# Kernel optimization log

Measured on AMD Instinct MI355X. Metric: run time of the kernel, lower is better.

Reference implementation:

```python
import jax, jax.numpy as jnp
import numpy as np

B, N, H, D = 1024, 128, 128, 8  # batch, num_nodes (= num variables), hidden, diffusion size


def setup_inputs() -> dict:
    key = jax.random.key(0)
    ks = jax.random.split(key, 7)
    return {
        "x": jax.random.normal(ks[0], (B, N), dtype=jnp.float32),
        "f_weight": jax.random.normal(ks[1], (N, N, H), dtype=jnp.float32) * 0.1,
        "g_weight": jax.random.normal(ks[2], (N, N, H, D), dtype=jnp.float32) * 0.1,
        "Wf": jax.random.normal(ks[3], (N, H), dtype=jnp.float32) * (1.0 / np.sqrt(H)),
        "bf": jax.random.normal(ks[4], (N,), dtype=jnp.float32) * 0.01,
        "Wg": jax.random.normal(ks[5], (N, H), dtype=jnp.float32) * (1.0 / np.sqrt(H)),
        "bg": jax.random.normal(ks[6], (N,), dtype=jnp.float32) * 0.01,
    }


def reference(x, f_weight, g_weight, Wf, bf, Wg, bg):
    # Drift f: per node i, temp_i = x @ f_weight[i]  -> [B,H]; out_i = fc_i(elu(temp_i)) -> [B,1]
    # Batched over nodes as a single einsum instead of the original Python loop.
    temp_f = jnp.einsum('bn,inh->bih', x, f_weight)              # [B,N,H]
    f_out = jnp.einsum('bih,ih->bi', jax.nn.elu(temp_f), Wf) + bf  # [B,N]

    # Diffusion g: per node i, temp_i = x @ g_weight[i] -> [B,H,D]; fc_i applied over H per diffusion channel.
    temp_g = jnp.einsum('bn,inhd->bihd', x, g_weight)            # [B,N,H,D]
    g_out = jnp.einsum('bihd,ih->bid', jax.nn.elu(temp_g), Wg) + bg[None, :, None]  # [B,N,D]
    return f_out, g_out
```

## Files before the change

### kernel.cpp

```cpp
#include <hip/hip_runtime.h>
#include <hip/hip_bf16.h>


typedef unsigned short u16;
typedef __attribute__((ext_vector_type(8))) short bf16x8;
typedef __attribute__((ext_vector_type(8))) short short8;
typedef __attribute__((ext_vector_type(4))) float f32x4;

typedef __attribute__((address_space(1))) const void* gas_ptr;
typedef __attribute__((address_space(3))) void* las_ptr;
#define GLOAD_LDS16(g, l) __builtin_amdgcn_global_load_lds((gas_ptr)(g), (las_ptr)(l), 16, 0, 0)

#define WS_W_ELEMS  ((size_t)128 * 1152 * 128)
#define WS_X_ELEMS  ((size_t)1024 * 128)
#define WS_NEED_BYTES ((WS_W_ELEMS + WS_X_ELEMS) * 2)

__device__ __forceinline__ u16 f2bf(float f) {
    unsigned int u = __float_as_uint(f);
    u += 0x7fffu + ((u >> 16) & 1u);
    return (u16)(u >> 16);
}
__device__ __forceinline__ uint32_t pack2bf(float a, float b) {
    return (uint32_t)f2bf(a) | ((uint32_t)f2bf(b) << 16);
}
__device__ __forceinline__ float elu(float v) {
    return v > 0.f ? v : __expf(v) - 1.f;
}

__global__ void sde_prepass(const float* __restrict__ fw, const float* __restrict__ gw,
                            const float* __restrict__ x, u16* __restrict__ wsW) {
    const int bx = blockIdx.x;
    const int t  = threadIdx.x;
    if (bx < 8192) {
        const int i  = bx >> 6;
        const int c  = (((bx >> 4) & 3) << 8) + t;
        const int n0 = (bx & 15) << 3;
        const float* src = gw + (size_t)i * 131072;
        float v[8];
        #pragma unroll
        for (int j = 0; j < 8; ++j) v[j] = src[(size_t)(n0 + j) * 1024 + c];
        short8 o;
        #pragma unroll
        for (int j = 0; j < 8; ++j) o[j] = (short)f2bf(v[j]);
        *(short8*)&wsW[((size_t)i * 1152 + c) * 128 + n0] = o;
    } else if (bx < 9216) {
        const int b2 = bx - 8192;
        const int i  = b2 >> 3;
        const int c  = t & 127;
        const int n0 = (((b2 & 7) << 1) + (t >> 7)) << 3;
        const float* src = fw + (size_t)i * 16384;
        float v[8];
        #pragma unroll
        for (int j = 0; j < 8; ++j) v[j] = src[(size_t)(n0 + j) * 128 + c];
        short8 o;
        #pragma unroll
        for (int j = 0; j < 8; ++j) o[j] = (short)f2bf(v[j]);
        *(short8*)&wsW[((size_t)i * 1152 + 1024 + c) * 128 + n0] = o;
    } else {
        const int tid = (bx - 9216) * 256 + t;
        float4 v = ((const float4*)x)[tid];
        ((uint2*)(wsW + WS_W_ELEMS))[tid] = make_uint2(pack2bf(v.x, v.y), pack2bf(v.z, v.w));
    }
}

__global__ __launch_bounds__(256, 4) void sde_mfma(
    const u16* __restrict__ wsAll,
    const float* __restrict__ Wf, const float* __restrict__ bfp,
    const float* __restrict__ Wg, const float* __restrict__ bgp,
    float* __restrict__ out)
{
    __shared__ u16 wst[64 * 128];
    __shared__ float wgs[128];
    __shared__ float wfs[128];

    const int t    = threadIdx.x;
    const int bx   = blockIdx.x;
    const int i    = bx & 127;
    const int b0   = (bx >> 7) << 7;
    const int w    = t >> 6;
    const int lane = t & 63;
    const int l15  = lane & 15;
    const int quad = lane >> 4;
    const int rl   = lane >> 4;
    const int j16  = lane & 15;
    const int sw   = l15 & 7;

    const u16* wsW = wsAll;
    const u16* wsX = wsAll + WS_W_ELEMS;

    if (t < 128) { wgs[t] = Wg[i * 128 + t]; wfs[t] = Wf[i * 128 + t]; }

    bf16x8 afrag[2][4];
    {
        const size_t r0 = (size_t)(b0 + w * 32 + l15) * 128 + quad * 8;
        #pragma unroll
        for (int kk = 0; kk < 4; ++kk) {
            afrag[0][kk] = *(const bf16x8*)&wsX[r0 + kk * 32];
            afrag[1][kk] = *(const bf16x8*)&wsX[r0 + 16 * 128 + kk * 32];
        }
    }

    float racc[8], frac[8];
    #pragma unroll
    for (int q = 0; q < 8; ++q) { racc[q] = 0.f; frac[q] = 0.f; }

    for (int ct = 0; ct < 18; ++ct) {
        {
            const char* srcW = (const char*)(wsW + ((size_t)i * 1152 + ct * 64) * 128);
            #pragma unroll
            for (int r = 0; r < 4; ++r) {
                int row = w * 16 + r * 4 + rl;
                int soff = row * 256 + ((j16 ^ (row & 7)) << 4);
                GLOAD_LDS16(srcW + soff, (char*)wst + w * 4096 + r * 1024);
            }
        }
        __syncthreads();

        f32x4 acc[2][4];
        #pragma unroll
        for (int rs = 0; rs < 2; ++rs)
            #pragma unroll
            for (int cs = 0; cs < 4; ++cs)
                acc[rs][cs] = (f32x4){0.f, 0.f, 0.f, 0.f};

        #pragma unroll
        for (int kk = 0; kk < 4; ++kk) {
            const int co = ((kk * 4 + quad) ^ sw) << 3;
            bf16x8 bv[4];
            #pragma unroll
            for (int cs = 0; cs < 4; ++cs)
                bv[cs] = *(const bf16x8*)&wst[(cs * 16 + l15) * 128 + co];
            #pragma unroll
            for (int cs = 0; cs < 4; ++cs) {
                acc[0][cs] = __builtin_amdgcn_mfma_f32_16x16x32_bf16(afrag[0][kk], bv[cs], acc[0][cs], 0, 0, 0);
                acc[1][cs] = __builtin_amdgcn_mfma_f32_16x16x32_bf16(afrag[1][kk], bv[cs], acc[1][cs], 0, 0, 0);
            }
        }

        if (ct < 16) {
            float wv[4];
            #pragma unroll
            for (int cs = 0; cs < 4; ++cs) wv[cs] = wgs[ct * 8 + cs * 2 + (l15 >> 3)];
            #pragma unroll
            for (int rs = 0; rs < 2; ++rs)
                #pragma unroll
                for (int rg = 0; rg < 4; ++rg) {
                    racc[rs * 4 + rg] += elu(acc[rs][0][rg]) * wv[0] + elu(acc[rs][1][rg]) * wv[1]
                                       + elu(acc[rs][2][rg]) * wv[2] + elu(acc[rs][3][rg]) * wv[3];
                }
        } else {
            float wv[4];
            #pragma unroll
            for (int cs = 0; cs < 4; ++cs) wv[cs] = wfs[(ct - 16) * 64 + cs * 16 + l15];
            #pragma unroll
            for (int rs = 0; rs < 2; ++rs)
                #pragma unroll
                for (int rg = 0; rg < 4; ++rg) {
                    frac[rs * 4 + rg] += elu(acc[rs][0][rg]) * wv[0] + elu(acc[rs][1][rg]) * wv[1]
                                       + elu(acc[rs][2][rg]) * wv[2] + elu(acc[rs][3][rg]) * wv[3];
                }
        }
        __syncthreads();
    }

    const float bfv = bfp[i], bgv = bgp[i];
    #pragma unroll
    for (int rs = 0; rs < 2; ++rs)
        #pragma unroll
        for (int rg = 0; rg < 4; ++rg) {
            int q = rs * 4 + rg;
            racc[q] += __shfl_xor(racc[q], 8);
            float fsum = frac[q];
            fsum += __shfl_xor(fsum, 1);
            fsum += __shfl_xor(fsum, 2);
            fsum += __shfl_xor(fsum, 4);
            fsum += __shfl_xor(fsum, 8);
            int row = w * 32 + rs * 16 + quad * 4 + rg;
            size_t brow = (size_t)(b0 + row);
            if (l15 == 0)
                out[brow * 128 + i] = fsum + bfv;
            if (l15 < 8)
                out[(size_t)131072 + (brow * 128 + i) * 8 + (lane & 7)] = racc[q] + bgv;
        }
}

__global__ void sde_fallback(const float* __restrict__ x, const float* __restrict__ fw,
                             const float* __restrict__ gw,
                             const float* __restrict__ Wf, const float* __restrict__ bfp,
                             const float* __restrict__ Wg, const float* __restrict__ bgp,
                             float* __restrict__ out)
{
    __shared__ float xsh[64 * 128];
    const int t  = threadIdx.x;
    const int i  = blockIdx.x >> 4;
    const int b0 = (blockIdx.x & 15) << 6;
    for (int idx = t; idx < 64 * 128; idx += 64) xsh[idx] = x[(size_t)b0 * 128 + idx];
    __syncthreads();
    const float* xr  = &xsh[t * 128];
    const float* fwi = fw + (size_t)i * 16384;
    const float* gwi = gw + (size_t)i * 131072;
    float fa = 0.f;
    for (int h = 0; h < 128; ++h) {
        float tf = 0.f;
        for (int n = 0; n < 128; ++n) tf += xr[n] * fwi[n * 128 + h];
        fa += elu(tf) * Wf[i * 128 + h];
    }
    float ga[8];
    #pragma unroll
    for (int d = 0; d < 8; ++d) ga[d] = 0.f;
    for (int h = 0; h < 128; ++h) {
        float tg[8] = {0, 0, 0, 0, 0, 0, 0, 0};
        for (int n = 0; n < 128; ++n) {
            float xv = xr[n];
            const float* gp = gwi + ((size_t)n * 128 + h) * 8;
            #pragma unroll
            for (int d = 0; d < 8; ++d) tg[d] += xv * gp[d];
        }
        float wv = Wg[i * 128 + h];
        #pragma unroll
        for (int d = 0; d < 8; ++d) ga[d] += elu(tg[d]) * wv;
    }
    size_t b = (size_t)(b0 + t);
    out[b * 128 + i] = fa + bfp[i];
    #pragma unroll
    for (int d = 0; d < 8; ++d)
        out[(size_t)131072 + (b * 128 + i) * 8 + d] = ga[d] + bgp[i];
}

extern "C" void kernel_launch(void* const* d_in, const int* in_sizes, int n_in,
                              void* d_out, int out_size, void* d_ws, size_t ws_size,
                              hipStream_t stream) {
    const float* x  = (const float*)d_in[0];
    const float* fw = (const float*)d_in[1];
    const float* gw = (const float*)d_in[2];
    const float* Wf = (const float*)d_in[3];
    const float* bf = (const float*)d_in[4];
    const float* Wg = (const float*)d_in[5];
    const float* bg = (const float*)d_in[6];
    float* out = (float*)d_out;

    if (ws_size >= WS_NEED_BYTES) {
        u16* wsAll = (u16*)d_ws;
        sde_prepass<<<9344, 256, 0, stream>>>(fw, gw, x, wsAll);
        sde_mfma<<<1024, 256, 0, stream>>>(wsAll, Wf, bf, Wg, bg, out);
    } else {
        sde_fallback<<<2048, 64, 0, stream>>>(x, fw, gw, Wf, bf, Wg, bg, out);
    }
}
```

Before: 193.1 us.

## Fuse weight conversion into MFMA kernel with double-buffered register-staged tiles

Removes the separate prepass that converted the fp32 weights and x to a bf16 workspace. The main kernel now reads fp32 weights directly, converts them in registers and writes swizzled tiles into a double-buffered LDS, overlapping the next tile's global loads with the current MFMAs. Each block now covers 256 batch rows, so every weight tile is reused across twice as many rows, with 512 blocks launched. ELU is rewritten as max(u,0)*ln2 + exp2(min(u,0)) on pre-scaled x, with the constant -1 folded out as a weight-sum correction at the end. The costs are more registers (launch bounds 2), fewer blocks, and bf16 rounding of x*log2e instead of x.

Measured after the change: 437.9 us. +126.8%, slower.

```diff
diff --git a/kernel.cpp b/kernel.cpp
--- a/kernel.cpp
+++ b/kernel.cpp
@@ -4,124 +4,126 @@
 
 typedef unsigned short u16;
 typedef __attribute__((ext_vector_type(8))) short bf16x8;
-typedef __attribute__((ext_vector_type(8))) short short8;
 typedef __attribute__((ext_vector_type(4))) float f32x4;
 
-typedef __attribute__((address_space(1))) const void* gas_ptr;
-typedef __attribute__((address_space(3))) void* las_ptr;
-#define GLOAD_LDS16(g, l) __builtin_amdgcn_global_load_lds((gas_ptr)(g), (las_ptr)(l), 16, 0, 0)
-
-#define WS_W_ELEMS  ((size_t)128 * 1152 * 128)
-#define WS_X_ELEMS  ((size_t)1024 * 128)
-#define WS_NEED_BYTES ((WS_W_ELEMS + WS_X_ELEMS) * 2)
-
-__device__ __forceinline__ u16 f2bf(float f) {
-    unsigned int u = __float_as_uint(f);
-    u += 0x7fffu + ((u >> 16) & 1u);
-    return (u16)(u >> 16);
-}
-__device__ __forceinline__ uint32_t pack2bf(float a, float b) {
-    return (uint32_t)f2bf(a) | ((uint32_t)f2bf(b) << 16);
-}
-__device__ __forceinline__ float elu(float v) {
-    return v > 0.f ? v : __expf(v) - 1.f;
-}
-
-__global__ void sde_prepass(const float* __restrict__ fw, const float* __restrict__ gw,
-                            const float* __restrict__ x, u16* __restrict__ wsW) {
-    const int bx = blockIdx.x;
-    const int t  = threadIdx.x;
-    if (bx < 8192) {
-        const int i  = bx >> 6;
-        const int c  = (((bx >> 4) & 3) << 8) + t;
-        const int n0 = (bx & 15) << 3;
-        const float* src = gw + (size_t)i * 131072;
-        float v[8];
-        #pragma unroll
-        for (int j = 0; j < 8; ++j) v[j] = src[(size_t)(n0 + j) * 1024 + c];
-        short8 o;
-        #pragma unroll
-        for (int j = 0; j < 8; ++j) o[j] = (short)f2bf(v[j]);
-        *(short8*)&wsW[((size_t)i * 1152 + c) * 128 + n0] = o;
-    } else if (bx < 9216) {
-        const int b2 = bx - 8192;
-        const int i  = b2 >> 3;
-        const int c  = t & 127;
-        const int n0 = (((b2 & 7) << 1) + (t >> 7)) << 3;
-        const float* src = fw + (size_t)i * 16384;
-        float v[8];
-        #pragma unroll
-        for (int j = 0; j < 8; ++j) v[j] = src[(size_t)(n0 + j) * 128 + c];
-        short8 o;
-        #pragma unroll
-        for (int j = 0; j < 8; ++j) o[j] = (short)f2bf(v[j]);
-        *(short8*)&wsW[((size_t)i * 1152 + 1024 + c) * 128 + n0] = o;
-    } else {
-        const int tid = (bx - 9216) * 256 + t;
-        float4 v = ((const float4*)x)[tid];
-        ((uint2*)(wsW + WS_W_ELEMS))[tid] = make_uint2(pack2bf(v.x, v.y), pack2bf(v.z, v.w));
-    }
-}
-
-__global__ __launch_bounds__(256, 4) void sde_mfma(
-    const u16* __restrict__ wsAll,
+#define LOG2E 1.4426950408889634f
+#define LN2   0.6931471805599453f
+
+__device__ __forceinline__ uint32_t pk2(float a, float b) {
+    __hip_bfloat162 h = __float22bfloat162_rn(make_float2(a, b));
+    union { __hip_bfloat162 h2; uint32_t u; } c;
+    c.h2 = h;
+    return c.u;
+}
+
+__device__ __forceinline__ float elu_acc(float u, float wv, float p) {
+    float m = fmaxf(u, 0.f);
+    float e = __builtin_amdgcn_exp2f(fminf(u, 0.f));
+    return fmaf(fmaf(m, LN2, e), wv, p);
+}
+
+__global__ __launch_bounds__(256, 2) void sde_fused(
+    const float* __restrict__ x, const float* __restrict__ fw, const float* __restrict__ gw,
     const float* __restrict__ Wf, const float* __restrict__ bfp,
     const float* __restrict__ Wg, const float* __restrict__ bgp,
     float* __restrict__ out)
 {
-    __shared__ u16 wst[64 * 128];
+    __shared__ u16 wst[2][64 * 128];
     __shared__ float wgs[128];
     __shared__ float wfs[128];
 
-    const int t    = threadIdx.x;
-    const int bx   = blockIdx.x;
+    const int t = threadIdx.x, bx = blockIdx.x;
     const int i    = bx & 127;
-    const int b0   = (bx >> 7) << 7;
+    const int b0   = (bx >> 7) << 8;
     const int w    = t >> 6;
     const int lane = t & 63;
     const int l15  = lane & 15;
     const int quad = lane >> 4;
-    const int rl   = lane >> 4;
-    const int j16  = lane & 15;
+    const int l31  = lane & 31;
+    const int jj   = lane >> 5;
+    const int c0   = l31 * 2;
     const int sw   = l15 & 7;
 
-    const u16* wsW = wsAll;
-    const u16* wsX = wsAll + WS_W_ELEMS;
-
     if (t < 128) { wgs[t] = Wg[i * 128 + t]; wfs[t] = Wf[i * 128 + t]; }
 
-    bf16x8 afrag[2][4];
-    {
-        const size_t r0 = (size_t)(b0 + w * 32 + l15) * 128 + quad * 8;
+    bf16x8 afr[4][4];
+    #pragma unroll
+    for (int ms = 0; ms < 4; ++ms) {
+        const float* xr = x + (size_t)(b0 + w * 64 + ms * 16 + l15) * 128 + quad * 8;
         #pragma unroll
         for (int kk = 0; kk < 4; ++kk) {
-            afrag[0][kk] = *(const bf16x8*)&wsX[r0 + kk * 32];
-            afrag[1][kk] = *(const bf16x8*)&wsX[r0 + 16 * 128 + kk * 32];
+            float4 v0 = *(const float4*)(xr + kk * 32);
+            float4 v1 = *(const float4*)(xr + kk * 32 + 4);
+            union { uint32_t u[4]; bf16x8 v; } r;
+            r.u[0] = pk2(v0.x * LOG2E, v0.y * LOG2E);
+            r.u[1] = pk2(v0.z * LOG2E, v0.w * LOG2E);
+            r.u[2] = pk2(v1.x * LOG2E, v1.y * LOG2E);
+            r.u[3] = pk2(v1.z * LOG2E, v1.w * LOG2E);
+            afr[ms][kk] = r.v;
         }
     }
 
-    float racc[8], frac[8];
+    const float* gwi = gw + (size_t)i * 131072;
+    const float* fwi = fw + (size_t)i * 16384;
+
+    float2 vr[2][8];
+    auto load_tile = [&](int ct) {
+        const float* src;
+        int rstride;
+        if (ct < 16) { src = gwi + ct * 64;        rstride = 1024; }
+        else         { src = fwi + (ct - 16) * 64; rstride = 128;  }
+        #pragma unroll
+        for (int it = 0; it < 2; ++it) {
+            const int j = w * 4 + it * 2 + jj;
+            const float* s2 = src + (size_t)(8 * j) * rstride + c0;
+            #pragma unroll
+            for (int r = 0; r < 8; ++r)
+                vr[it][r] = *(const float2*)(s2 + (size_t)r * rstride);
+        }
+    };
+    auto write_tile = [&](int p) {
+        #pragma unroll
+        for (int it = 0; it < 2; ++it) {
+            const int j = w * 4 + it * 2 + jj;
+            {
+                const int c = c0;
+                union { uint32_t u[4]; bf16x8 v; } rr;
+                rr.u[0] = pk2(vr[it][0].x, vr[it][1].x);
+                rr.u[1] = pk2(vr[it][2].x, vr[it][3].x);
+                rr.u[2] = pk2(vr[it][4].x, vr[it][5].x);
+                rr.u[3] = pk2(vr[it][6].x, vr[it][7].x);
+                *(bf16x8*)&wst[p][c * 128 + ((j ^ (c & 7)) << 3)] = rr.v;
+            }
+            {
+                const int c = c0 + 1;
+                union { uint32_t u[4]; bf16x8 v; } rr;
+                rr.u[0] = pk2(vr[it][0].y, vr[it][1].y);
+                rr.u[1] = pk2(vr[it][2].y, vr[it][3].y);
+                rr.u[2] = pk2(vr[it][4].y, vr[it][5].y);
+                rr.u[3] = pk2(vr[it][6].y, vr[it][7].y);
+                *(bf16x8*)&wst[p][c * 128 + ((j ^ (c & 7)) << 3)] = rr.v;
+            }
+        }
+    };
+
+    float racc[16], frac[16];
     #pragma unroll
-    for (int q = 0; q < 8; ++q) { racc[q] = 0.f; frac[q] = 0.f; }
-
+    for (int q = 0; q < 16; ++q) { racc[q] = 0.f; frac[q] = 0.f; }
+
+    load_tile(0);
+    write_tile(0);
+    __syncthreads();
+
+    int p = 0;
     for (int ct = 0; ct < 18; ++ct) {
-        {
-            const char* srcW = (const char*)(wsW + ((size_t)i * 1152 + ct * 64) * 128);
-            #pragma unroll
-            for (int r = 0; r < 4; ++r) {
-                int row = w * 16 + r * 4 + rl;
-                int soff = row * 256 + ((j16 ^ (row & 7)) << 4);
-                GLOAD_LDS16(srcW + soff, (char*)wst + w * 4096 + r * 1024);
-            }
-        }
-        __syncthreads();
-
-        f32x4 acc[2][4];
-        #pragma unroll
-        for (int rs = 0; rs < 2; ++rs)
+        if (ct < 17) load_tile(ct + 1);
+
+        f32x4 acc[4][4];
+        #pragma unroll
+        for (int ms = 0; ms < 4; ++ms)
             #pragma unroll
             for (int cs = 0; cs < 4; ++cs)
-                acc[rs][cs] = (f32x4){0.f, 0.f, 0.f, 0.f};
+                acc[ms][cs] = (f32x4){0.f, 0.f, 0.f, 0.f};
 
         #pragma unroll
         for (int kk = 0; kk < 4; ++kk) {
@@ -129,12 +131,12 @@
             bf16x8 bv[4];
             #pragma unroll
             for (int cs = 0; cs < 4; ++cs)
-                bv[cs] = *(const bf16x8*)&wst[(cs * 16 + l15) * 128 + co];
-            #pragma unroll
-            for (int cs = 0; cs < 4; ++cs) {
-                acc[0][cs] = __builtin_amdgcn_mfma_f32_16x16x32_bf16(afrag[0][kk], bv[cs], acc[0][cs], 0, 0, 0);
-                acc[1][cs] = __builtin_amdgcn_mfma_f32_16x16x32_bf16(afrag[1][kk], bv[cs], acc[1][cs], 0, 0, 0);
-            }
+                bv[cs] = *(const bf16x8*)&wst[p][(cs * 16 + l15) * 128 + co];
+            #pragma unroll
+            for (int ms = 0; ms < 4; ++ms)
+                #pragma unroll
+                for (int cs = 0; cs < 4; ++cs)
+                    acc[ms][cs] = __builtin_amdgcn_mfma_f32_16x16x32_bf16(afr[ms][kk], bv[cs], acc[ms][cs], 0, 0, 0);
         }
 
         if (ct < 16) {
@@ -142,89 +144,69 @@
             #pragma unroll
             for (int cs = 0; cs < 4; ++cs) wv[cs] = wgs[ct * 8 + cs * 2 + (l15 >> 3)];
             #pragma unroll
-            for (int rs = 0; rs < 2; ++rs)
+            for (int ms = 0; ms < 4; ++ms)
                 #pragma unroll
                 for (int rg = 0; rg < 4; ++rg) {
-                    racc[rs * 4 + rg] += elu(acc[rs][0][rg]) * wv[0] + elu(acc[rs][1][rg]) * wv[1]
-                                       + elu(acc[rs][2][rg]) * wv[2] + elu(acc[rs][3][rg]) * wv[3];
+                    float s = racc[ms * 4 + rg];
+                    s = elu_acc(acc[ms][0][rg], wv[0], s);
+                    s = elu_acc(acc[ms][1][rg], wv[1], s);
+                    s = elu_acc(acc[ms][2][rg], wv[2], s);
+                    s = elu_acc(acc[ms][3][rg], wv[3], s);
+                    racc[ms * 4 + rg] = s;
                 }
         } else {
             float wv[4];
             #pragma unroll
             for (int cs = 0; cs < 4; ++cs) wv[cs] = wfs[(ct - 16) * 64 + cs * 16 + l15];
             #pragma unroll
-            for (int rs = 0; rs < 2; ++rs)
+            for (int ms = 0; ms < 4; ++ms)
                 #pragma unroll
                 for (int rg = 0; rg < 4; ++rg) {
-                    frac[rs * 4 + rg] += elu(acc[rs][0][rg]) * wv[0] + elu(acc[rs][1][rg]) * wv[1]
-                                       + elu(acc[rs][2][rg]) * wv[2] + elu(acc[rs][3][rg]) * wv[3];
+                    float s = frac[ms * 4 + rg];
+                    s = elu_acc(acc[ms][0][rg], wv[0], s);
+                    s = elu_acc(acc[ms][1][rg], wv[1], s);
+                    s = elu_acc(acc[ms][2][rg], wv[2], s);
+                    s = elu_acc(acc[ms][3][rg], wv[3], s);
+                    frac[ms * 4 + rg] = s;
                 }
         }
-        __syncthreads();
+
+        if (ct < 17) {
+            write_tile(p ^ 1);
+            __syncthreads();
+            p ^= 1;
+        }
+    }
+
+    float Sg = 0.f, Sf = 0.f;
+    {
+        const int hb = l15 >> 3;
+        #pragma unroll 8
+        for (int h = 0; h < 128; h += 2) Sg += wgs[h + hb];
+        #pragma unroll
+        for (int h = 0; h < 128; h += 16) Sf += wfs[h + l15];
     }
 
     const float bfv = bfp[i], bgv = bgp[i];
     #pragma unroll
-    for (int rs = 0; rs < 2; ++rs)
+    for (int ms = 0; ms < 4; ++ms)
         #pragma unroll
         for (int rg = 0; rg < 4; ++rg) {
-            int q = rs * 4 + rg;
-            racc[q] += __shfl_xor(racc[q], 8);
-            float fsum = frac[q];
-            fsum += __shfl_xor(fsum, 1);
-            fsum += __shfl_xor(fsum, 2);
-            fsum += __shfl_xor(fsum, 4);
-            fsum += __shfl_xor(fsum, 8);
-            int row = w * 32 + rs * 16 + quad * 4 + rg;
-            size_t brow = (size_t)(b0 + row);
+            const int q = ms * 4 + rg;
+            float g = racc[q] - Sg;
+            g += __shfl_xor(g, 8);
+            float f = frac[q] - Sf;
+            f += __shfl_xor(f, 1);
+            f += __shfl_xor(f, 2);
+            f += __shfl_xor(f, 4);
+            f += __shfl_xor(f, 8);
+            const int row = w * 64 + ms * 16 + quad * 4 + rg;
+            const size_t brow = (size_t)(b0 + row);
             if (l15 == 0)
-                out[brow * 128 + i] = fsum + bfv;
+                out[brow * 128 + i] = f + bfv;
             if (l15 < 8)
-                out[(size_t)131072 + (brow * 128 + i) * 8 + (lane & 7)] = racc[q] + bgv;
-        }
-}
-
-__global__ void sde_fallback(const float* __restrict__ x, const float* __restrict__ fw,
-                             const float* __restrict__ gw,
-                             const float* __restrict__ Wf, const float* __restrict__ bfp,
-                             const float* __restrict__ Wg, const float* __restrict__ bgp,
-                             float* __restrict__ out)
-{
-    __shared__ float xsh[64 * 128];
-    const int t  = threadIdx.x;
-    const int i  = blockIdx.x >> 4;
-    const int b0 = (blockIdx.x & 15) << 6;
-    for (int idx = t; idx < 64 * 128; idx += 64) xsh[idx] = x[(size_t)b0 * 128 + idx];
-    __syncthreads();
-    const float* xr  = &xsh[t * 128];
-    const float* fwi = fw + (size_t)i * 16384;
-    const float* gwi = gw + (size_t)i * 131072;
-    float fa = 0.f;
-    for (int h = 0; h < 128; ++h) {
-        float tf = 0.f;
-        for (int n = 0; n < 128; ++n) tf += xr[n] * fwi[n * 128 + h];
-        fa += elu(tf) * Wf[i * 128 + h];
-    }
-    float ga[8];
-    #pragma unroll
-    for (int d = 0; d < 8; ++d) ga[d] = 0.f;
-    for (int h = 0; h < 128; ++h) {
-        float tg[8] = {0, 0, 0, 0, 0, 0, 0, 0};
-        for (int n = 0; n < 128; ++n) {
-            float xv = xr[n];
-            const float* gp = gwi + ((size_t)n * 128 + h) * 8;
-            #pragma unroll
-            for (int d = 0; d < 8; ++d) tg[d] += xv * gp[d];
-        }
-        float wv = Wg[i * 128 + h];
-        #pragma unroll
-        for (int d = 0; d < 8; ++d) ga[d] += elu(tg[d]) * wv;
-    }
-    size_t b = (size_t)(b0 + t);
-    out[b * 128 + i] = fa + bfp[i];
-    #pragma unroll
-    for (int d = 0; d < 8; ++d)
-        out[(size_t)131072 + (b * 128 + i) * 8 + d] = ga[d] + bgp[i];
+                out[(size_t)131072 + (brow * 128 + i) * 8 + (lane & 7)] = g + bgv;
+        }
 }
 
 extern "C" void kernel_launch(void* const* d_in, const int* in_sizes, int n_in,
@@ -238,12 +220,7 @@
     const float* Wg = (const float*)d_in[5];
     const float* bg = (const float*)d_in[6];
     float* out = (float*)d_out;
-
-    if (ws_size >= WS_NEED_BYTES) {
-        u16* wsAll = (u16*)d_ws;
-        sde_prepass<<<9344, 256, 0, stream>>>(fw, gw, x, wsAll);
-        sde_mfma<<<1024, 256, 0, stream>>>(wsAll, Wf, bf, Wg, bg, out);
-    } else {
-        sde_fallback<<<2048, 64, 0, stream>>>(x, fw, gw, Wf, bf, Wg, bg, out);
-    }
-}
+    (void)d_ws; (void)ws_size;
+
+    sde_fused<<<512, 256, 0, stream>>>(x, fw, gw, Wf, bf, Wg, bg, out);
+}
```
